# Kernel optimization log

Measured on AMD Instinct MI355X. Metric: run time of the kernel, lower is better.

The kernel has to match this reference:

```python
import jax, jax.numpy as jnp
import numpy as np

NUM_ORI = 4
VM_R, VM_RG = 10.0, 15.0
B_INH, G_INH = 1.5, 1.0
VM_W, VM_W2 = 0.1, 0.4
VM_WG, VM_W2G = 0.2, 0.4
BORDER_K = 11   # int(10*1.1)=11, already odd
GROUP_K = 23    # int(15*1.5)=22 -> +1 to make odd


def create_von_mises(size, r0, theta0, centered, w, w2):
    x = np.arange(size) - size / 2
    y = -(np.arange(size) - size / 2)
    X, Y = np.meshgrid(x, y)
    if centered:
        X = X + r0 * np.cos(theta0)
        Y = Y + r0 * np.sin(theta0)
    r = np.sqrt(X ** 2 + Y ** 2)
    th = np.arctan2(Y, X)
    # np.i0 == scipy.special.iv(0, .) for real args (I0 is even)
    return np.exp(r0 * w * np.cos(th - theta0)) / np.i0(w2 * (r - r0))


def make_filters():
    borders, groups = [], []
    for ori in np.arange(0.0, 180.0, 180.0 / NUM_ORI):
        a = ori * np.pi / 180.0
        b = (ori + 180.0) * np.pi / 180.0
        borders.append(create_von_mises(BORDER_K, VM_R, a, True, VM_W, VM_W2))
        borders.append(create_von_mises(BORDER_K, VM_R, b, True, VM_W, VM_W2))
        g1 = create_von_mises(GROUP_K, VM_RG, a, False, VM_W, VM_W2)
        g2 = create_von_mises(GROUP_K, VM_RG, b, False, VM_WG, VM_W2G)
        groups += [g1, g1, g2, g2]
    # only border filters are normalized to [-1, 1] in the original code
    borders = [f / (f.max() / 2.0) - 1.0 for f in borders]
    Wb = np.stack(borders)[:, None].astype(np.float32)   # [2*O, 1, 11, 11]
    Wg = np.stack(groups)[:, None].astype(np.float32)    # [4*O, 1, 23, 23]
    return jnp.asarray(Wb), jnp.asarray(Wg)


def setup_inputs() -> dict:
    key = jax.random.key(0)
    inp = jax.random.uniform(key, (4, 2, 512, 512), dtype=jnp.float32)
    Wb, Wg = make_filters()
    return {"inp": inp, "W_border": Wb, "W_group": Wg}


def _conv(x, w, pad, groups):
    return jax.lax.conv_general_dilated(
        x, w, (1, 1), [(pad, pad), (pad, pad)],
        dimension_numbers=("NCHW", "OIHW", "NCHW"),
        feature_group_count=groups)


def _spike(v):
    # LIF with tau_mem=0.01, zero initial v_mem, single step: alpha=exp(-1/tau)~0,
    # so v_mem = input; spike when v_mem >= threshold (1.0).
    return (v >= 1.0).astype(v.dtype)


def reference(inp, W_border, W_group):
    B, _, H, W = inp.shape
    pad_b = (BORDER_K - 1) // 2
    pad_g = (GROUP_K - 1) // 2
    # border ownership: conv each polarity with the 8 von-Mises filters + LIF
    pos = _spike(_conv(inp[:, 0:1], W_border, pad_b, 1))  # [B, 2*O, H, W]
    neg = _spike(_conv(inp[:, 1:2], W_border, pad_b, 1))
    vmap_ = inp.sum(1)[:, None]                           # [B, 1, H, W]
    pe, po = pos[:, 0::2], pos[:, 1::2]   # even=ori, odd=opposite ori
    ne, no = neg[:, 0::2], neg[:, 1::2]
    b13 = _spike(vmap_ * (pe - no * B_INH)) + _spike(vmap_ * (ne - po * B_INH))
    b24 = _spike(vmap_ * (po - ne * B_INH)) + _spike(vmap_ * (no - pe * B_INH))
    # winner-take-all over orientations
    diff = b13 - b24                                      # [B, O, H, W]
    tp = jnp.abs(diff)
    wta = jax.lax.stop_gradient(
        (tp == tp.max(axis=1, keepdims=True)).astype(inp.dtype))
    b1p = _spike(wta * diff)
    b1n = _spike(-(wta * diff))
    # channel order is ori-major: [t1_o, t2_o, t3_o, t4_o] per orientation
    border = jnp.stack(
        [b1p * b13, b1p * b24 * G_INH, b1n * b24, b1n * b13 * G_INH],
        axis=2).reshape(B, 4 * NUM_ORI, H, W)
    g = _spike(_conv(border, W_group, pad_g, 4 * NUM_ORI))
    g = g.reshape(B, NUM_ORI, 4, H, W)
    return (_spike(g[:, :, 0] - g[:, :, 1])
            + _spike(g[:, :, 2] - g[:, :, 3])).sum(1)     # [B, H, W]
```

## Files before the change

kernel.cpp:

```cpp
#include <hip/hip_runtime.h>

#define HH 512
#define WW 512
#define NB 4

#define K1 11
#define PAD1 5
#define T1X 32
#define T1Y 16
#define IN1X 42
#define IN1Y 26
#define S1 44

__device__ __forceinline__ unsigned conv8_pass2(const float* __restrict__ sm,
                                                const float* __restrict__ Wb,
                                                int py, int px)
{
    float acc[8][2];
    #pragma unroll
    for (int c = 0; c < 8; c++) { acc[c][0] = 0.f; acc[c][1] = 0.f; }

    #pragma unroll 1
    for (int ky = 0; ky < K1; ky++) {
        const float2* rp = (const float2*)&sm[(py + ky) * S1 + px];
        float a[12];
        #pragma unroll
        for (int r = 0; r < 6; r++) *(float2*)&a[2 * r] = rp[r];
        #pragma unroll
        for (int c = 0; c < 8; c++) {
            #pragma unroll
            for (int kx = 0; kx < K1; kx++) {
                const float wv = Wb[c * 121 + ky * 11 + kx];
                acc[c][0] = fmaf(a[kx],     wv, acc[c][0]);
                acc[c][1] = fmaf(a[kx + 1], wv, acc[c][1]);
            }
        }
    }
    unsigned bits = 0;
    #pragma unroll
    for (int c = 0; c < 8; c++) {
        bits |= (acc[c][0] >= 1.f ? 1u : 0u) << (c * 2);
        bits |= (acc[c][1] >= 1.f ? 1u : 0u) << (c * 2 + 1);
    }
    return bits;
}

__global__ __launch_bounds__(256, 8) void stage1_kernel(
    const float* __restrict__ inp, const float* __restrict__ Wb,
    unsigned char* __restrict__ border)
{
    __shared__ __align__(16) float s0[IN1Y * S1];
    __shared__ __align__(16) float s1[IN1Y * S1];

    const int b   = blockIdx.z;
    const int tx0 = blockIdx.x * T1X;
    const int ty0 = blockIdx.y * T1Y;
    const float* in0 = inp + ((size_t)b * 2 + 0) * (HH * WW);
    const float* in1 = inp + ((size_t)b * 2 + 1) * (HH * WW);

    for (int i = threadIdx.x; i < IN1Y * IN1X; i += 256) {
        int iy = i / IN1X, ix = i - iy * IN1X;
        int gy = ty0 + iy - PAD1, gx = tx0 + ix - PAD1;
        bool ok = (gy >= 0) & (gy < HH) & (gx >= 0) & (gx < WW);
        int idx = gy * WW + gx;
        s0[iy * S1 + ix] = ok ? in0[idx] : 0.f;
        s1[iy * S1 + ix] = ok ? in1[idx] : 0.f;
    }
    __syncthreads();

    const int lx = threadIdx.x & 15;
    const int ly = threadIdx.x >> 4;
    const int px = lx * 2;
    const int py = ly;

    const unsigned bitP = conv8_pass2(s0, Wb, py, px);
    const unsigned bitN = conv8_pass2(s1, Wb, py, px);

    const int gy = ty0 + py;
    const int gxbase = tx0 + px;

    float vm[2];
    #pragma unroll
    for (int p = 0; p < 2; p++)
        vm[p] = s0[(py + PAD1) * S1 + px + PAD1 + p]
              + s1[(py + PAD1) * S1 + px + PAD1 + p];

    float b13[4][2], b24[4][2];
    #pragma unroll
    for (int o = 0; o < 4; o++) {
        #pragma unroll
        for (int p = 0; p < 2; p++) {
            float pe = (float)((bitP >> (4 * o + p))     & 1u);
            float po = (float)((bitP >> (4 * o + 2 + p)) & 1u);
            float ne = (float)((bitN >> (4 * o + p))     & 1u);
            float no = (float)((bitN >> (4 * o + 2 + p)) & 1u);
            float sa = (vm[p] * (pe - 1.5f * no) >= 1.f) ? 1.f : 0.f;
            float sb = (vm[p] * (ne - 1.5f * po) >= 1.f) ? 1.f : 0.f;
            b13[o][p] = sa + sb;
            float sc = (vm[p] * (po - 1.5f * ne) >= 1.f) ? 1.f : 0.f;
            float sd = (vm[p] * (no - 1.5f * pe) >= 1.f) ? 1.f : 0.f;
            b24[o][p] = sc + sd;
        }
    }
    float mxp[2];
    #pragma unroll
    for (int p = 0; p < 2; p++) {
        float m = 0.f;
        #pragma unroll
        for (int o = 0; o < 4; o++) m = fmaxf(m, fabsf(b13[o][p] - b24[o][p]));
        mxp[p] = m;
    }
    #pragma unroll
    for (int o = 0; o < 4; o++) {
        unsigned short w0 = 0, w1 = 0, w2 = 0, w3 = 0;
        #pragma unroll
        for (int p = 0; p < 2; p++) {
            float d   = b13[o][p] - b24[o][p];
            float wta = (fabsf(d) == mxp[p]) ? 1.f : 0.f;
            float b1p = (wta * d >= 1.f)    ? 1.f : 0.f;
            float b1n = (-(wta * d) >= 1.f) ? 1.f : 0.f;
            w0 |= (unsigned short)(unsigned char)(b1p * b13[o][p]) << (8 * p);
            w1 |= (unsigned short)(unsigned char)(b1p * b24[o][p]) << (8 * p);
            w2 |= (unsigned short)(unsigned char)(b1n * b24[o][p]) << (8 * p);
            w3 |= (unsigned short)(unsigned char)(b1n * b13[o][p]) << (8 * p);
        }
        size_t base = (((size_t)b * 16 + 4 * o) * HH + gy) * WW + gxbase;
        *(unsigned short*)&border[base]                       = w0;
        *(unsigned short*)&border[base + (size_t)HH * WW]     = w1;
        *(unsigned short*)&border[base + (size_t)2 * HH * WW] = w2;
        *(unsigned short*)&border[base + (size_t)3 * HH * WW] = w3;
    }
}

#define K2 23
#define PAD2 11
#define T2X 32
#define T2Y 128
#define SROW 18
#define R2 150

__device__ __forceinline__ float ubyte_f(unsigned dw, int byi) {
    return (float)((dw >> (8 * byi)) & 0xffu);
}

__global__ __launch_bounds__(256, 4) void stage2_kernel(
    const unsigned char* __restrict__ border, const float* __restrict__ Wg,
    unsigned char* __restrict__ gsp)
{
    __shared__ unsigned tile[R2 * SROW];

    const int z   = blockIdx.z;
    const int b   = z >> 4;
    const int c   = z & 15;
    const int tx0 = blockIdx.x * T2X;
    const int ty0 = blockIdx.y * T2Y;
    const unsigned char* bp = border + ((size_t)b * 16 + c) * (HH * WW);

    for (int i = threadIdx.x; i < R2 * 16; i += 256) {
        int iy = i >> 4, cc = i & 15;
        int gy  = ty0 - PAD2 + iy;
        int gx0 = tx0 - 12 + 4 * cc;
        unsigned u = 0;
        if (((unsigned)gy < HH) & ((unsigned)gx0 < WW))
            u = *(const unsigned*)(bp + (size_t)gy * WW + gx0);
        tile[iy * SROW + cc] = u;
    }
    __syncthreads();

    const int lx = threadIdx.x & 3;
    const int ly = threadIdx.x >> 2;
    const int px = lx * 8;
    const int py = ly * 2;

    float acc[2][8];
    #pragma unroll
    for (int dy = 0; dy < 2; dy++)
        #pragma unroll
        for (int p = 0; p < 8; p++) acc[dy][p] = 0.f;

    const float* wc = Wg + c * (K2 * K2);

    #pragma unroll 1
    for (int kyb = 0; kyb < 7; kyb++) {
        const int b0 = kyb * 3;
        #pragma unroll
        for (int r = 0; r < 4; r++) {
            const int trow = py + b0 + r;
            unsigned d[8];
            const uint2* tp2 = (const uint2*)&tile[trow * SROW + 2 * lx];
            #pragma unroll
            for (int r2 = 0; r2 < 4; r2++) { uint2 v = tp2[r2]; d[2*r2] = v.x; d[2*r2+1] = v.y; }
            float a[31];
            #pragma unroll
            for (int j = 1; j <= 30; j++) a[j] = ubyte_f(d[j >> 2], j & 3);
            #pragma unroll
            for (int jk = 0; jk < 3; jk++) {
                const int dy = r - jk;
                if (dy >= 0 && dy < 2) {
                    #pragma unroll
                    for (int kx = 0; kx < 23; kx++) {
                        const float wv = wc[(b0 + jk) * 23 + kx];
                        #pragma unroll
                        for (int p = 0; p < 8; p++)
                            acc[dy][p] = fmaf(a[p + kx + 1], wv, acc[dy][p]);
                    }
                }
            }
        }
    }
    {
        const int b0 = 21;
        #pragma unroll
        for (int r = 0; r < 3; r++) {
            const int trow = py + b0 + r;
            unsigned d[8];
            const uint2* tp2 = (const uint2*)&tile[trow * SROW + 2 * lx];
            #pragma unroll
            for (int r2 = 0; r2 < 4; r2++) { uint2 v = tp2[r2]; d[2*r2] = v.x; d[2*r2+1] = v.y; }
            float a[31];
            #pragma unroll
            for (int j = 1; j <= 30; j++) a[j] = ubyte_f(d[j >> 2], j & 3);
            #pragma unroll
            for (int jk = 0; jk < 2; jk++) {
                const int dy = r - jk;
                if (dy >= 0 && dy < 2) {
                    #pragma unroll
                    for (int kx = 0; kx < 23; kx++) {
                        const float wv = wc[(b0 + jk) * 23 + kx];
                        #pragma unroll
                        for (int p = 0; p < 8; p++)
                            acc[dy][p] = fmaf(a[p + kx + 1], wv, acc[dy][p]);
                    }
                }
            }
        }
    }

    const int ox = tx0 + px;
    unsigned char* gp = gsp + ((size_t)b * 16 + c) * (HH * WW);
    #pragma unroll
    for (int dy = 0; dy < 2; dy++) {
        const int oy = ty0 + py + dy;
        unsigned lo = 0, hi = 0;
        #pragma unroll
        for (int p = 0; p < 4; p++) lo |= (acc[dy][p]     >= 1.f ? 1u : 0u) << (8 * p);
        #pragma unroll
        for (int p = 0; p < 4; p++) hi |= (acc[dy][p + 4] >= 1.f ? 1u : 0u) << (8 * p);
        uint2 v; v.x = lo; v.y = hi;
        *(uint2*)&gp[(size_t)oy * WW + ox] = v;
    }
}

__global__ __launch_bounds__(256) void combine_kernel(
    const unsigned char* __restrict__ gsp, float* __restrict__ out)
{
    const int idx = blockIdx.x * 256 + threadIdx.x;
    const int b = idx >> 16;
    const int r = idx & 65535;
    const unsigned* g = (const unsigned*)gsp;
    const int pb = b * 16;
    unsigned s = 0;
    #pragma unroll
    for (int o = 0; o < 4; o++) {
        unsigned g0 = g[(size_t)(pb + 4 * o + 0) * 65536 + r];
        unsigned g1 = g[(size_t)(pb + 4 * o + 1) * 65536 + r];
        unsigned g2 = g[(size_t)(pb + 4 * o + 2) * 65536 + r];
        unsigned g3 = g[(size_t)(pb + 4 * o + 3) * 65536 + r];
        s += ((g0 & ~g1) & 0x01010101u) + ((g2 & ~g3) & 0x01010101u);
    }
    float4 f;
    f.x = (float)(s & 255u);
    f.y = (float)((s >> 8) & 255u);
    f.z = (float)((s >> 16) & 255u);
    f.w = (float)(s >> 24);
    ((float4*)out)[idx] = f;
}

extern "C" void kernel_launch(void* const* d_in, const int* in_sizes, int n_in,
                              void* d_out, int out_size, void* d_ws, size_t ws_size,
                              hipStream_t stream)
{
    const float* inp = (const float*)d_in[0];
    const float* Wb  = (const float*)d_in[1];
    const float* Wg  = (const float*)d_in[2];
    unsigned char* border = (unsigned char*)d_ws;
    unsigned char* gsp    = border + (size_t)NB * 16 * HH * WW;
    float* out = (float*)d_out;

    dim3 blk(256);
    dim3 g1(WW / T1X, HH / T1Y, NB);
    stage1_kernel<<<g1, blk, 0, stream>>>(inp, Wb, border);
    dim3 g2(WW / T2X, HH / T2Y, NB * 16);
    stage2_kernel<<<g2, blk, 0, stream>>>(border, Wg, gsp);
    dim3 g3((NB * HH * WW / 4) / 256);
    combine_kernel<<<g3, blk, 0, stream>>>(gsp, out);
}
```

Before: 289.4 us.

## Compute four output rows per thread in group conv and swizzle shared tile

The stage-2 group convolution now has each thread produce four output rows instead of two, with the tile height doubled to 256 rows so one loaded input row feeds up to four accumulators. This cuts shared-memory loads and byte-to-float conversions per output. The shared tile uses an XOR swizzle on the column index to reduce bank conflicts from the wider row stride between threads. In exchange there are more registers (32 accumulators), a larger shared tile that may lower occupancy, and a runtime-bounded loop with in-loop branches over kernel rows.

```diff
diff --git a/kernel.cpp b/kernel.cpp
--- a/kernel.cpp
+++ b/kernel.cpp
@@ -135,9 +135,9 @@
 #define K2 23
 #define PAD2 11
 #define T2X 32
-#define T2Y 128
+#define T2Y 256
 #define SROW 18
-#define R2 150
+#define R2 278
 
 __device__ __forceinline__ float ubyte_f(unsigned dw, int byi) {
     return (float)((dw >> (8 * byi)) & 0xffu);
@@ -163,83 +163,56 @@
         unsigned u = 0;
         if (((unsigned)gy < HH) & ((unsigned)gx0 < WW))
             u = *(const unsigned*)(bp + (size_t)gy * WW + gx0);
-        tile[iy * SROW + cc] = u;
+        tile[iy * SROW + (cc ^ ((iy >> 3) & 6))] = u;
     }
     __syncthreads();
 
     const int lx = threadIdx.x & 3;
     const int ly = threadIdx.x >> 2;
     const int px = lx * 8;
-    const int py = ly * 2;
-
-    float acc[2][8];
-    #pragma unroll
-    for (int dy = 0; dy < 2; dy++)
+    const int py = ly * 4;
+
+    float acc[4][8];
+    #pragma unroll
+    for (int dy = 0; dy < 4; dy++)
         #pragma unroll
         for (int p = 0; p < 8; p++) acc[dy][p] = 0.f;
 
     const float* wc = Wg + c * (K2 * K2);
 
     #pragma unroll 1
-    for (int kyb = 0; kyb < 7; kyb++) {
-        const int b0 = kyb * 3;
-        #pragma unroll
-        for (int r = 0; r < 4; r++) {
-            const int trow = py + b0 + r;
-            unsigned d[8];
-            const uint2* tp2 = (const uint2*)&tile[trow * SROW + 2 * lx];
-            #pragma unroll
-            for (int r2 = 0; r2 < 4; r2++) { uint2 v = tp2[r2]; d[2*r2] = v.x; d[2*r2+1] = v.y; }
-            float a[31];
-            #pragma unroll
-            for (int j = 1; j <= 30; j++) a[j] = ubyte_f(d[j >> 2], j & 3);
-            #pragma unroll
-            for (int jk = 0; jk < 3; jk++) {
-                const int dy = r - jk;
-                if (dy >= 0 && dy < 2) {
+    for (int t = 0; t < K2 + 3; t++) {
+        const int trow = py + t;
+        const int sw = (trow >> 3) & 6;
+        unsigned d[8];
+        #pragma unroll
+        for (int r2 = 0; r2 < 4; r2++) {
+            uint2 v = *(const uint2*)&tile[trow * SROW + ((2 * (lx + r2)) ^ sw)];
+            d[2 * r2] = v.x; d[2 * r2 + 1] = v.y;
+        }
+        float a[31];
+        #pragma unroll
+        for (int j = 1; j <= 30; j++) a[j] = ubyte_f(d[j >> 2], j & 3);
+        #pragma unroll
+        for (int dy = 0; dy < 4; dy++) {
+            const int ky = t - dy;
+            if (ky >= 0 && ky < K2) {
+                const float* wr = wc + ky * K2;
+                #pragma unroll
+                for (int kx = 0; kx < 23; kx++) {
+                    const float wv = wr[kx];
                     #pragma unroll
-                    for (int kx = 0; kx < 23; kx++) {
-                        const float wv = wc[(b0 + jk) * 23 + kx];
-                        #pragma unroll
-                        for (int p = 0; p < 8; p++)
-                            acc[dy][p] = fmaf(a[p + kx + 1], wv, acc[dy][p]);
-                    }
+                    for (int p = 0; p < 8; p++)
+                        acc[dy][p] = fmaf(a[p + kx + 1], wv, acc[dy][p]);
                 }
             }
         }
     }
-    {
-        const int b0 = 21;
-        #pragma unroll
-        for (int r = 0; r < 3; r++) {
-            const int trow = py + b0 + r;
-            unsigned d[8];
-            const uint2* tp2 = (const uint2*)&tile[trow * SROW + 2 * lx];
-            #pragma unroll
-            for (int r2 = 0; r2 < 4; r2++) { uint2 v = tp2[r2]; d[2*r2] = v.x; d[2*r2+1] = v.y; }
-            float a[31];
-            #pragma unroll
-            for (int j = 1; j <= 30; j++) a[j] = ubyte_f(d[j >> 2], j & 3);
-            #pragma unroll
-            for (int jk = 0; jk < 2; jk++) {
-                const int dy = r - jk;
-                if (dy >= 0 && dy < 2) {
-                    #pragma unroll
-                    for (int kx = 0; kx < 23; kx++) {
-                        const float wv = wc[(b0 + jk) * 23 + kx];
-                        #pragma unroll
-                        for (int p = 0; p < 8; p++)
-                            acc[dy][p] = fmaf(a[p + kx + 1], wv, acc[dy][p]);
-                    }
-                }
-            }
-        }
-    }
 
     const int ox = tx0 + px;
     unsigned char* gp = gsp + ((size_t)b * 16 + c) * (HH * WW);
     #pragma unroll
-    for (int dy = 0; dy < 2; dy++) {
+    for (int dy = 0; dy < 4; dy++) {
         const int oy = ty0 + py + dy;
         unsigned lo = 0, hi = 0;
         #pragma unroll
```

Result: no change. 284.1 us (-1.8%).
